# Optimization experiments

Hardware: AMD Instinct MI355X
Metric: run time of the kernel (lower is better)

Reference implementation:

```python
import jax, jax.numpy as jnp
import numpy as np
import math

D_MODEL = 1024
N_HEADS = 16
DK = D_MODEL // N_HEADS


def setup_inputs() -> dict:
    key = jax.random.key(0)
    kx, kqkv, kproj = jax.random.split(key, 3)
    B, T = 4, 2048
    x = jax.random.normal(kx, (B, T, D_MODEL), dtype=jnp.float32)
    # torch Linear weight is [out, in]; y = x @ W.T
    W_qkv = jax.random.normal(kqkv, (3 * D_MODEL, D_MODEL), dtype=jnp.float32) * (1.0 / math.sqrt(D_MODEL))
    W_proj = jax.random.normal(kproj, (D_MODEL, D_MODEL), dtype=jnp.float32) * (1.0 / math.sqrt(D_MODEL))
    return {"x": x, "W_qkv": W_qkv, "W_proj": W_proj}


def reference(x, W_qkv, W_proj):
    B, T, D = x.shape
    qkv = jnp.einsum("btd,ed->bte", x, W_qkv)  # [B,T,3D]
    q, k, v = jnp.split(qkv, 3, axis=-1)
    # [B,T,D] -> [B,H,T,dk]
    def heads(t):
        return t.reshape(B, T, N_HEADS, DK).transpose(0, 2, 1, 3)
    q, k, v = heads(q), heads(k), heads(v)
    scale = 1.0 / math.sqrt(DK)
    att = jnp.einsum("bhqd,bhkd->bhqk", q, k) * scale  # [B,H,T,T]
    att = jax.nn.softmax(att, axis=-1)
    out = jnp.einsum("bhqk,bhkd->bhqd", att, v)  # [B,H,T,dk]
    out = out.transpose(0, 2, 1, 3).reshape(B, T, D)
    return jnp.einsum("btd,ed->bte", out, W_proj)
```

## Files before the change

kernel.cpp:

```cpp
#include <hip/hip_runtime.h>
#include <hip/hip_bf16.h>

#define D_MODEL 1024
#define N_HEADS 16
#define DK 64
#define B_SZ 4
#define T_SEQ 2048
#define M_ROWS (B_SZ * T_SEQ)
#define QK_SCALE_LOG2 0.18033688f

typedef short bf16x8 __attribute__((ext_vector_type(8)));
typedef float f32x4  __attribute__((ext_vector_type(4)));

__device__ inline unsigned short f32_to_bf16(float f) {
    union { float f; unsigned int u; } v; v.f = f;
    unsigned int r = v.u + 0x7fff + ((v.u >> 16) & 1);
    return (unsigned short)(r >> 16);
}
__device__ inline unsigned int pack_bf16x2(float a, float b) {
    __hip_bfloat162 t = __float22bfloat162_rn(make_float2(a, b));
    union { __hip_bfloat162 v; unsigned int u; } c; c.v = t;
    return c.u;
}

__global__ __launch_bounds__(256) void cast_bf16(
    const float* __restrict__ src, unsigned short* __restrict__ dst,
    int n, int nscaled, float s)
{
    for (int i = (blockIdx.x * 256 + threadIdx.x) * 4; i < n;
         i += gridDim.x * 256 * 4) {
        float4 v = *(const float4*)(src + i);
        const float sc = (i < nscaled) ? s : 1.0f;
        ushort4 h;
        h.x = f32_to_bf16(v.x * sc); h.y = f32_to_bf16(v.y * sc);
        h.z = f32_to_bf16(v.z * sc); h.w = f32_to_bf16(v.w * sc);
        *(ushort4*)(dst + i) = h;
    }
}

template <typename OutT>
__global__ __launch_bounds__(256, 4) void gemm_bf16_nt(
    const unsigned short* __restrict__ A, const unsigned short* __restrict__ B,
    OutT* __restrict__ C, int M, int N, int K, int nbx)
{
    __shared__ __align__(16) unsigned short sA[128 * 64];
    __shared__ __align__(16) unsigned short sB[128 * 64];

    const int t    = threadIdx.x;
    const int wave = t >> 6;
    const int lane = t & 63;
    const int l15  = lane & 15;
    const int quad = lane >> 4;
    const int swz  = l15 & 7;

    const int cpx = gridDim.x >> 3;
    const int wg  = (blockIdx.x & 7) * cpx + (blockIdx.x >> 3);
    const int n0  = (wg % nbx) * 128;
    const int m0  = (wg / nbx) * 128;

    const unsigned short* gplane = (wave < 2) ? A : B;
    unsigned short* lplane = (wave < 2) ? sA : sB;
    const int row0 = ((wave < 2) ? m0 : n0) + (wave & 1) * 64;
    unsigned short* lbase = lplane + (wave & 1) * 4096;
    const int rsub = lane >> 3;
    const int cg   = (lane & 7) ^ rsub;
    const unsigned short* gbase =
        gplane + (size_t)(row0 + rsub) * K + cg * 8;

    f32x4 acc[4][4];
#pragma unroll
    for (int i = 0; i < 4; ++i)
#pragma unroll
        for (int j = 0; j < 4; ++j) acc[i][j] = (f32x4){0.f, 0.f, 0.f, 0.f};

    const int wr = (wave >> 1) * 64;
    const int wc = (wave & 1) * 64;

    for (int k0 = 0; k0 < K; k0 += 64) {
#pragma unroll
        for (int i = 0; i < 8; ++i) {
            __builtin_amdgcn_global_load_lds(
                (const __attribute__((address_space(1))) unsigned int*)
                    (gbase + k0 + (size_t)(i * 8) * K),
                (__attribute__((address_space(3))) unsigned int*)
                    (lbase + i * 512),
                16, 0, 0);
        }
        __syncthreads();

#pragma unroll
        for (int kk = 0; kk < 2; ++kk) {
            bf16x8 a[4], b[4];
            const int ch = kk * 4 + quad;
            const int co = (ch ^ swz) * 8;
#pragma unroll
            for (int f = 0; f < 4; ++f) {
                a[f] = *(const bf16x8*)&sA[(wr + f * 16 + l15) * 64 + co];
                b[f] = *(const bf16x8*)&sB[(wc + f * 16 + l15) * 64 + co];
            }
#pragma unroll
            for (int mi = 0; mi < 4; ++mi)
#pragma unroll
                for (int ni = 0; ni < 4; ++ni)
                    acc[mi][ni] = __builtin_amdgcn_mfma_f32_16x16x32_bf16(
                        a[mi], b[ni], acc[mi][ni], 0, 0, 0);
        }
        __syncthreads();
    }

#pragma unroll
    for (int mi = 0; mi < 4; ++mi)
#pragma unroll
        for (int r = 0; r < 4; ++r) {
            OutT* crow =
                C + (size_t)(m0 + wr + mi * 16 + quad * 4 + r) * N + n0 + wc + l15;
#pragma unroll
            for (int ni = 0; ni < 4; ++ni) {
                if constexpr (sizeof(OutT) == 2)
                    crow[ni * 16] = (OutT)f32_to_bf16(acc[mi][ni][r]);
                else
                    crow[ni * 16] = (OutT)acc[mi][ni][r];
            }
        }
}

__global__ __launch_bounds__(256) void prep_vt(
    const unsigned short* __restrict__ qkvb, unsigned short* __restrict__ vt)
{
    __shared__ unsigned short VT_s[64][132];
    const int t  = threadIdx.x;
    const int b  = blockIdx.z, h = blockIdx.y;
    const int t0 = blockIdx.x * 128;
    const unsigned short* vb = qkvb + (size_t)(b * T_SEQ) * (3 * D_MODEL)
                               + 2 * D_MODEL + h * DK;
#pragma unroll
    for (int it = 0; it < 8; ++it) {
        const int trow = (t >> 4) + it * 16;
        const int dk0  = (t & 15) * 4;
        ushort4 v = *(const ushort4*)(vb + (size_t)(t0 + trow) * (3 * D_MODEL) + dk0);
        VT_s[dk0 + 0][trow] = v.x; VT_s[dk0 + 1][trow] = v.y;
        VT_s[dk0 + 2][trow] = v.z; VT_s[dk0 + 3][trow] = v.w;
    }
    __syncthreads();

    const int c     = t >> 4;
    const int p8    = c * 8;
    const int sbase = (p8 & ~31) + ((p8 >> 3) & 3) * 4;
    unsigned short* dst =
        vt + (((size_t)((b * N_HEADS + h) * (T_SEQ / 128) + blockIdx.x) * 16 + c)
              * 64) * 8;
#pragma unroll
    for (int dd = 0; dd < 4; ++dd) {
        const int d = (t & 15) + dd * 16;
        ushort4 a  = *(const ushort4*)&VT_s[d][sbase];
        ushort4 b4 = *(const ushort4*)&VT_s[d][sbase + 16];
        union { ushort4 p[2]; uint4 v; } pk;
        pk.p[0] = a; pk.p[1] = b4;
        *(uint4*)(dst + d * 8) = pk.v;
    }
}

__global__ __launch_bounds__(256, 4) void attn_mfma(
    const unsigned short* __restrict__ qkvb,
    const unsigned short* __restrict__ vt,
    unsigned short* __restrict__ ob)
{
    __shared__ __align__(16) unsigned short Ksw[2][128 * 64];

    const int t    = threadIdx.x;
    const int wave = t >> 6;
    const int lane = t & 63;
    const int l15  = t & 15;
    const int quad = lane >> 4;
    const int swz  = l15 & 7;

    const int b  = blockIdx.z;
    const int h  = blockIdx.y;
    const int q0 = blockIdx.x * 128;

    bf16x8 qa[2][2];
#pragma unroll
    for (int qs = 0; qs < 2; ++qs) {
        const unsigned short* qrow =
            qkvb + ((size_t)(b * T_SEQ) + q0 + wave * 32 + qs * 16 + l15)
                   * (3 * D_MODEL) + h * DK;
        qa[qs][0] = *(const bf16x8*)(qrow + quad * 8);
        qa[qs][1] = *(const bf16x8*)(qrow + 32 + quad * 8);
    }

    f32x4 O[2][4], Lacc[2];
#pragma unroll
    for (int qs = 0; qs < 2; ++qs) {
        Lacc[qs] = (f32x4){0.f, 0.f, 0.f, 0.f};
#pragma unroll
        for (int nd = 0; nd < 4; ++nd) O[qs][nd] = (f32x4){0.f, 0.f, 0.f, 0.f};
    }

    const short one_bf = (short)0x3F80;
    const bf16x8 ones8 = {one_bf, one_bf, one_bf, one_bf,
                          one_bf, one_bf, one_bf, one_bf};

    const unsigned short* kbase =
        qkvb + (size_t)(b * T_SEQ) * (3 * D_MODEL) + D_MODEL + h * DK;
    const unsigned short* vbase =
        vt + (size_t)(b * N_HEADS + h) * DK * T_SEQ;

    const int krl  = wave * 32 + (lane >> 3);
    const int kcol = ((lane & 7) ^ (lane >> 3)) * 8;

#pragma unroll
    for (int i = 0; i < 4; ++i) {
        const int rk = krl + i * 8;
        __builtin_amdgcn_global_load_lds(
            (const __attribute__((address_space(1))) unsigned int*)
                (kbase + (size_t)rk * (3 * D_MODEL) + kcol),
            (__attribute__((address_space(3))) unsigned int*)
                (&Ksw[0][(wave * 4 + i) * 512]),
            16, 0, 0);
    }

    const int NT = T_SEQ / 128;
    for (int tile = 0; tile < NT; ++tile) {
        __syncthreads();

        if (tile + 1 < NT) {
            const int c0n = (tile + 1) * 128;
            const int nb  = (tile + 1) & 1;
#pragma unroll
            for (int i = 0; i < 4; ++i) {
                const int rk = krl + i * 8;
                __builtin_amdgcn_global_load_lds(
                    (const __attribute__((address_space(1))) unsigned int*)
                        (kbase + (size_t)(c0n + rk) * (3 * D_MODEL) + kcol),
                    (__attribute__((address_space(3))) unsigned int*)
                        (&Ksw[nb][(wave * 4 + i) * 512]),
                    16, 0, 0);
            }
        }

        const int cb = tile & 1;
        const unsigned short* vtile = vbase + (size_t)tile * (16 * 64 * 8);
        const unsigned short* vlane = vtile + quad * 512 + l15 * 8;
#pragma unroll
        for (int half = 0; half < 2; ++half) {
            f32x4 S[2][4];
#pragma unroll
            for (int qs = 0; qs < 2; ++qs)
#pragma unroll
                for (int nf = 0; nf < 4; ++nf) S[qs][nf] = (f32x4){0.f, 0.f, 0.f, 0.f};

            __builtin_amdgcn_s_setprio(1);
#pragma unroll
            for (int ks = 0; ks < 2; ++ks) {
                const int ch = ks * 4 + quad;
#pragma unroll
                for (int nf = 0; nf < 4; ++nf) {
                    const int row = half * 64 + nf * 16 + l15;
                    const bf16x8 kf =
                        *(const bf16x8*)&Ksw[cb][row * 64 + ((ch ^ swz) * 8)];
                    S[0][nf] = __builtin_amdgcn_mfma_f32_16x16x32_bf16(
                        kf, qa[0][ks], S[0][nf], 0, 0, 0);
                    S[1][nf] = __builtin_amdgcn_mfma_f32_16x16x32_bf16(
                        kf, qa[1][ks], S[1][nf], 0, 0, 0);
                }
            }
            __builtin_amdgcn_s_setprio(0);

#pragma unroll
            for (int gl = 0; gl < 2; ++gl) {
                bf16x8 pf[2];
#pragma unroll
                for (int qs = 0; qs < 2; ++qs) {
                    union { uint4 u; bf16x8 v; } cv;
                    const f32x4 s0 = S[qs][2 * gl];
                    const f32x4 s1 = S[qs][2 * gl + 1];
                    cv.u.x = pack_bf16x2(__builtin_amdgcn_exp2f(s0[0]),
                                         __builtin_amdgcn_exp2f(s0[1]));
                    cv.u.y = pack_bf16x2(__builtin_amdgcn_exp2f(s0[2]),
                                         __builtin_amdgcn_exp2f(s0[3]));
                    cv.u.z = pack_bf16x2(__builtin_amdgcn_exp2f(s1[0]),
                                         __builtin_amdgcn_exp2f(s1[1]));
                    cv.u.w = pack_bf16x2(__builtin_amdgcn_exp2f(s1[2]),
                                         __builtin_amdgcn_exp2f(s1[3]));
                    pf[qs] = cv.v;
                }
                const int g = half * 2 + gl;
                const unsigned short* vptr = vlane + (size_t)g * 2048;
                __builtin_amdgcn_s_setprio(1);
#pragma unroll
                for (int nd = 0; nd < 4; ++nd) {
                    const bf16x8 vb = *(const bf16x8*)(vptr + nd * 128);
                    O[0][nd] = __builtin_amdgcn_mfma_f32_16x16x32_bf16(
                        pf[0], vb, O[0][nd], 0, 0, 0);
                    O[1][nd] = __builtin_amdgcn_mfma_f32_16x16x32_bf16(
                        pf[1], vb, O[1][nd], 0, 0, 0);
                }
                Lacc[0] = __builtin_amdgcn_mfma_f32_16x16x32_bf16(
                    pf[0], ones8, Lacc[0], 0, 0, 0);
                Lacc[1] = __builtin_amdgcn_mfma_f32_16x16x32_bf16(
                    pf[1], ones8, Lacc[1], 0, 0, 0);
                __builtin_amdgcn_s_setprio(0);
            }
        }
    }

#pragma unroll
    for (int qs = 0; qs < 2; ++qs)
#pragma unroll
        for (int r = 0; r < 4; ++r) {
            const float invl = 1.0f / Lacc[qs][r];
            const size_t rowbase =
                ((size_t)(b * T_SEQ) + q0 + wave * 32 + qs * 16 + quad * 4 + r)
                * D_MODEL + h * DK + l15;
#pragma unroll
            for (int nd = 0; nd < 4; ++nd)
                ob[rowbase + nd * 16] = f32_to_bf16(O[qs][nd][r] * invl);
        }
}

extern "C" void kernel_launch(void* const* d_in, const int* in_sizes, int n_in,
                              void* d_out, int out_size, void* d_ws, size_t ws_size,
                              hipStream_t stream)
{
    const float* x      = (const float*)d_in[0];
    const float* W_qkv  = (const float*)d_in[1];
    const float* W_proj = (const float*)d_in[2];
    float* out = (float*)d_out;

    const size_t XN = (size_t)M_ROWS * D_MODEL;
    const size_t WQ = (size_t)3 * D_MODEL * D_MODEL;
    const size_t WP = (size_t)D_MODEL * D_MODEL;
    unsigned short* xb   = (unsigned short*)d_ws;
    unsigned short* wqb  = xb + XN;
    unsigned short* wpb  = wqb + WQ;
    unsigned short* qkvb = wpb + WP;
    unsigned short* vtb  = qkvb + (size_t)M_ROWS * 3 * D_MODEL;
    unsigned short* ab   = xb;

    dim3 blk(256);
    cast_bf16<<<512, blk, 0, stream>>>(x, xb, (int)XN, 0, 1.0f);
    cast_bf16<<<256, blk, 0, stream>>>(W_qkv, wqb, (int)WQ,
                                       D_MODEL * D_MODEL, QK_SCALE_LOG2);
    cast_bf16<<<128, blk, 0, stream>>>(W_proj, wpb, (int)WP, 0, 1.0f);

    gemm_bf16_nt<unsigned short>
        <<<dim3((3 * D_MODEL / 128) * (M_ROWS / 128)), blk, 0, stream>>>(
        xb, wqb, qkvb, M_ROWS, 3 * D_MODEL, D_MODEL, 3 * D_MODEL / 128);

    prep_vt<<<dim3(T_SEQ / 128, N_HEADS, B_SZ), blk, 0, stream>>>(qkvb, vtb);
    attn_mfma<<<dim3(T_SEQ / 128, N_HEADS, B_SZ), blk, 0, stream>>>(
        qkvb, vtb, ab);

    gemm_bf16_nt<float>
        <<<dim3((D_MODEL / 128) * (M_ROWS / 128)), blk, 0, stream>>>(
        ab, wpb, out, M_ROWS, D_MODEL, D_MODEL, D_MODEL / 128);
}
```

Baseline: 275.6 us.

## Fuse V transpose into QKV GEMM epilogue and merge cast kernels

```diff
diff --git a/kernel.cpp b/kernel.cpp
--- a/kernel.cpp
+++ b/kernel.cpp
@@ -9,6 +9,10 @@
 #define M_ROWS (B_SZ * T_SEQ)
 #define QK_SCALE_LOG2 0.18033688f
 
+#define XN ((size_t)M_ROWS * D_MODEL)
+#define WQ ((size_t)3 * D_MODEL * D_MODEL)
+#define WP ((size_t)D_MODEL * D_MODEL)
+
 typedef short bf16x8 __attribute__((ext_vector_type(8)));
 typedef float f32x4  __attribute__((ext_vector_type(4)));
 
@@ -23,25 +27,38 @@
     return c.u;
 }
 
-__global__ __launch_bounds__(256) void cast_bf16(
-    const float* __restrict__ src, unsigned short* __restrict__ dst,
-    int n, int nscaled, float s)
+__global__ __launch_bounds__(256) void cast_all(
+    const float* __restrict__ x, const float* __restrict__ W_qkv,
+    const float* __restrict__ W_proj,
+    unsigned short* __restrict__ xb, unsigned short* __restrict__ wqb,
+    unsigned short* __restrict__ wpb)
 {
-    for (int i = (blockIdx.x * 256 + threadIdx.x) * 4; i < n;
-         i += gridDim.x * 256 * 4) {
-        float4 v = *(const float4*)(src + i);
-        const float sc = (i < nscaled) ? s : 1.0f;
+    const size_t total = (XN + WQ + WP) / 4;
+    for (size_t i4 = blockIdx.x * 256 + threadIdx.x; i4 < total;
+         i4 += gridDim.x * 256) {
+        const size_t i = i4 * 4;
+        const float* src; unsigned short* dst; float sc = 1.0f; size_t off;
+        if (i < XN) {
+            src = x; dst = xb; off = i;
+        } else if (i < XN + WQ) {
+            off = i - XN; src = W_qkv; dst = wqb;
+            if (off < (size_t)D_MODEL * D_MODEL) sc = QK_SCALE_LOG2;
+        } else {
+            off = i - XN - WQ; src = W_proj; dst = wpb;
+        }
+        float4 v = *(const float4*)(src + off);
         ushort4 h;
         h.x = f32_to_bf16(v.x * sc); h.y = f32_to_bf16(v.y * sc);
         h.z = f32_to_bf16(v.z * sc); h.w = f32_to_bf16(v.w * sc);
-        *(ushort4*)(dst + i) = h;
-    }
-}
-
-template <typename OutT>
+        *(ushort4*)(dst + off) = h;
+    }
+}
+
+template <typename OutT, bool FUSE_VT>
 __global__ __launch_bounds__(256, 4) void gemm_bf16_nt(
     const unsigned short* __restrict__ A, const unsigned short* __restrict__ B,
-    OutT* __restrict__ C, int M, int N, int K, int nbx)
+    OutT* __restrict__ C, unsigned short* __restrict__ vt,
+    int M, int N, int K, int nbx)
 {
     __shared__ __align__(16) unsigned short sA[128 * 64];
     __shared__ __align__(16) unsigned short sB[128 * 64];
@@ -108,6 +125,34 @@
         __syncthreads();
     }
 
+    if constexpr (FUSE_VT) {
+        if (n0 >= 2 * D_MODEL) {
+            const int bb   = m0 >> 11;
+            const int tile = (m0 & 2047) >> 7;
+            const int hA   = (n0 + wc - 2 * D_MODEL) >> 6;
+            unsigned short* vtile =
+                vt + ((size_t)((bb * N_HEADS + hA) * (T_SEQ / 128) + tile))
+                     * (16 * 64 * 8);
+            const int chi = (wr >> 6) * 8;
+#pragma unroll
+            for (int cc = 0; cc < 2; ++cc) {
+                const int c   = chi + cc * 4 + quad;
+                const int mi0 = 2 * cc;
+#pragma unroll
+                for (int ni = 0; ni < 4; ++ni) {
+                    const int d = ni * 16 + l15;
+                    uint4 p;
+                    p.x = pack_bf16x2(acc[mi0][ni][0],     acc[mi0][ni][1]);
+                    p.y = pack_bf16x2(acc[mi0][ni][2],     acc[mi0][ni][3]);
+                    p.z = pack_bf16x2(acc[mi0 + 1][ni][0], acc[mi0 + 1][ni][1]);
+                    p.w = pack_bf16x2(acc[mi0 + 1][ni][2], acc[mi0 + 1][ni][3]);
+                    *(uint4*)(vtile + (c * 64 + d) * 8) = p;
+                }
+            }
+            return;
+        }
+    }
+
 #pragma unroll
     for (int mi = 0; mi < 4; ++mi)
 #pragma unroll
@@ -122,42 +167,6 @@
                     crow[ni * 16] = (OutT)acc[mi][ni][r];
             }
         }
-}
-
-__global__ __launch_bounds__(256) void prep_vt(
-    const unsigned short* __restrict__ qkvb, unsigned short* __restrict__ vt)
-{
-    __shared__ unsigned short VT_s[64][132];
-    const int t  = threadIdx.x;
-    const int b  = blockIdx.z, h = blockIdx.y;
-    const int t0 = blockIdx.x * 128;
-    const unsigned short* vb = qkvb + (size_t)(b * T_SEQ) * (3 * D_MODEL)
-                               + 2 * D_MODEL + h * DK;
-#pragma unroll
-    for (int it = 0; it < 8; ++it) {
-        const int trow = (t >> 4) + it * 16;
-        const int dk0  = (t & 15) * 4;
-        ushort4 v = *(const ushort4*)(vb + (size_t)(t0 + trow) * (3 * D_MODEL) + dk0);
-        VT_s[dk0 + 0][trow] = v.x; VT_s[dk0 + 1][trow] = v.y;
-        VT_s[dk0 + 2][trow] = v.z; VT_s[dk0 + 3][trow] = v.w;
-    }
-    __syncthreads();
-
-    const int c     = t >> 4;
-    const int p8    = c * 8;
-    const int sbase = (p8 & ~31) + ((p8 >> 3) & 3) * 4;
-    unsigned short* dst =
-        vt + (((size_t)((b * N_HEADS + h) * (T_SEQ / 128) + blockIdx.x) * 16 + c)
-              * 64) * 8;
-#pragma unroll
-    for (int dd = 0; dd < 4; ++dd) {
-        const int d = (t & 15) + dd * 16;
-        ushort4 a  = *(const ushort4*)&VT_s[d][sbase];
-        ushort4 b4 = *(const ushort4*)&VT_s[d][sbase + 16];
-        union { ushort4 p[2]; uint4 v; } pk;
-        pk.p[0] = a; pk.p[1] = b4;
-        *(uint4*)(dst + d * 8) = pk.v;
-    }
 }
 
 __global__ __launch_bounds__(256, 4) void attn_mfma(
@@ -327,9 +336,6 @@
     const float* W_proj = (const float*)d_in[2];
     float* out = (float*)d_out;
 
-    const size_t XN = (size_t)M_ROWS * D_MODEL;
-    const size_t WQ = (size_t)3 * D_MODEL * D_MODEL;
-    const size_t WP = (size_t)D_MODEL * D_MODEL;
     unsigned short* xb   = (unsigned short*)d_ws;
     unsigned short* wqb  = xb + XN;
     unsigned short* wpb  = wqb + WQ;
@@ -338,20 +344,16 @@
     unsigned short* ab   = xb;
 
     dim3 blk(256);
-    cast_bf16<<<512, blk, 0, stream>>>(x, xb, (int)XN, 0, 1.0f);
-    cast_bf16<<<256, blk, 0, stream>>>(W_qkv, wqb, (int)WQ,
-                                       D_MODEL * D_MODEL, QK_SCALE_LOG2);
-    cast_bf16<<<128, blk, 0, stream>>>(W_proj, wpb, (int)WP, 0, 1.0f);
-
-    gemm_bf16_nt<unsigned short>
+    cast_all<<<1024, blk, 0, stream>>>(x, W_qkv, W_proj, xb, wqb, wpb);
+
+    gemm_bf16_nt<unsigned short, true>
         <<<dim3((3 * D_MODEL / 128) * (M_ROWS / 128)), blk, 0, stream>>>(
-        xb, wqb, qkvb, M_ROWS, 3 * D_MODEL, D_MODEL, 3 * D_MODEL / 128);
-
-    prep_vt<<<dim3(T_SEQ / 128, N_HEADS, B_SZ), blk, 0, stream>>>(qkvb, vtb);
+        xb, wqb, qkvb, vtb, M_ROWS, 3 * D_MODEL, D_MODEL, 3 * D_MODEL / 128);
+
     attn_mfma<<<dim3(T_SEQ / 128, N_HEADS, B_SZ), blk, 0, stream>>>(
         qkvb, vtb, ab);
 
-    gemm_bf16_nt<float>
+    gemm_bf16_nt<float, false>
         <<<dim3((D_MODEL / 128) * (M_ROWS / 128)), blk, 0, stream>>>(
-        ab, wpb, out, M_ROWS, D_MODEL, D_MODEL, D_MODEL / 128);
-}
+        ab, wpb, out, nullptr, M_ROWS, D_MODEL, D_MODEL, D_MODEL / 128);
+}
```

Measured after the change: 264.6 us. -4.0%, faster.
